# Performance work log

Hardware: AMD Instinct MI355X
Metric: run time of the kernel (lower is better)

The kernel has to match this reference:

```python
import jax, jax.numpy as jnp
import numpy as np
from jax import lax

B, T, DEPTH = 512, 32, 512
RNN, NCC = 512, 128
D_IN = DEPTH * (T * DEPTH // T // DEPTH) * 1 + NCC  # slice_len=1 -> 512 + 128 = 640


def setup_inputs() -> dict:
    key = jax.random.key(0)
    ks = jax.random.split(key, 7)
    s = 0.05  # tf.random_normal_initializer default stddev
    return {
        "f_pool": jax.random.normal(ks[0], (B, T, DEPTH), jnp.float32),
        "ground_truth": jax.random.normal(ks[1], (B, T, NCC), jnp.float32),
        "kernel": jax.random.normal(ks[2], (DEPTH + NCC, 4 * RNN), jnp.float32) * s,
        "rec_kernel": jax.random.normal(ks[3], (RNN, 4 * RNN), jnp.float32) * s,
        "bias": jax.random.normal(ks[4], (4 * RNN,), jnp.float32) * s,
        "softmax_w": jax.random.normal(ks[5], (RNN, NCC), jnp.float32) * s,
        "softmax_b": jax.random.normal(ks[6], (NCC,), jnp.float32) * s,
    }


def reference(f_pool, ground_truth, kernel, rec_kernel, bias, softmax_w, softmax_b):
    b, features_num, depth = f_pool.shape
    seq_length = ground_truth.shape[1]
    ncc = softmax_b.shape[0]
    rnn = rec_kernel.shape[0]
    slice_len = features_num // seq_length  # == 1 here
    gt_t = jnp.transpose(ground_truth, (1, 0, 2))  # [T, B, C] for scan

    def step(carry, inp):
        h, c, prev = carry
        t, gt_row = inp
        # image feature slice at char index t -> [B, slice_len*depth]
        feat = lax.dynamic_slice_in_dim(f_pool, t, slice_len, axis=1)
        feat = feat.reshape(b, slice_len * depth)
        x = jnp.concatenate([feat, prev], axis=1)
        z = x @ kernel + h @ rec_kernel + bias  # [B, 4*rnn]
        i, f, g, o = jnp.split(z, 4, axis=1)    # keras LSTMCell gate order
        c2 = jax.nn.sigmoid(f) * c + jax.nn.sigmoid(i) * jnp.tanh(g)
        h2 = jax.nn.sigmoid(o) * jnp.tanh(c2)
        logits = h2 @ softmax_w + softmax_b
        onehot = jax.nn.one_hot(jnp.argmax(logits, axis=1), ncc, dtype=f_pool.dtype)
        # teacher forcing: prev_output = ground_truth[:, t, :]
        return (h2, c2, gt_row), onehot

    h0 = jnp.zeros((b, rnn), f_pool.dtype)
    c0 = jnp.zeros((b, rnn), f_pool.dtype)
    prev0 = jnp.zeros((b, ncc), f_pool.dtype)
    (h, c, _), outs = lax.scan(step, (h0, c0, prev0), (jnp.arange(seq_length), gt_t))
    sequence_output = jnp.transpose(outs, (1, 0, 2))  # [B, T, C]
    return (sequence_output, h, c)
```

## Files before the change

kernel.cpp:

```cpp
#include <hip/hip_runtime.h>
#include <math.h>

typedef float  f32x4  __attribute__((ext_vector_type(4)));
typedef short  short8v __attribute__((ext_vector_type(8)));
typedef unsigned short ushort8v __attribute__((ext_vector_type(8)));
typedef unsigned short ushort4v __attribute__((ext_vector_type(4)));

#define KP_PRE 3840
#define KP_HS  1536

#define WAITV(N) asm volatile("s_waitcnt vmcnt(" #N ")" ::: "memory")
#define SBAR()   asm volatile("s_barrier" ::: "memory")

__device__ unsigned short g_Xb[16384][3840];
__device__ unsigned short g_Wb[2048][3840];
__device__ unsigned short g_Rb[2048][1536];
__device__ unsigned short g_hs[2][512][1536];
__device__ float g_pre[16384][2048];
__device__ float g_hf[2][512 * 512];
__device__ float g_swT[128][512];
__device__ float g_bperm[2048];
__device__ float g_plv[2][512 * 8];
__device__ int   g_pli[2][512 * 8];
__device__ unsigned g_xcnt[128];
__device__ unsigned g_pcnt[256];
__device__ unsigned g_prel[256];

__global__ void init_counters()
{
    int t = threadIdx.x;
    if (t < 8) g_xcnt[t * 16] = 0u;
    if (t < 4) { g_pcnt[t * 64] = 0u; g_prel[t * 64] = 0u; }
}

__device__ __forceinline__ unsigned short f2bf(float f) {
    unsigned u = __float_as_uint(f);
    return (unsigned short)((u + 0x7fffu + ((u >> 16) & 1u)) >> 16);
}
__device__ __forceinline__ float bf2f(unsigned short s) {
    return __uint_as_float(((unsigned)s) << 16);
}
__device__ __forceinline__ float sigf(float x) { return 1.f / (1.f + expf(-x)); }

__device__ __forceinline__ void split3(float v, unsigned short& s0,
                                       unsigned short& s1, unsigned short& s2) {
    s0 = f2bf(v); float f0 = bf2f(s0);
    s1 = f2bf(v - f0); float f1 = bf2f(s1);
    s2 = f2bf(v - f0 - f1);
}

__device__ __constant__ int c_ipt[6] = {0, 0, 1, 0, 1, 2};
__device__ __constant__ int c_jpt[6] = {0, 1, 0, 2, 1, 0};

__device__ __forceinline__ void gl16(const unsigned short* g, unsigned short* l) {
    __builtin_amdgcn_global_load_lds((const __attribute__((address_space(1))) void*)g,
                                     (__attribute__((address_space(3))) void*)l, 16, 0, 0);
}

__device__ __forceinline__ short8v fragld(const unsigned short* sh, int row, int uw) {
    return *(const short8v*)(sh + row * 64 + ((uw ^ (row & 7)) << 3));
}

template<int AUNITS, int BUNITS>
__device__ __forceinline__ void stage_chunk(const unsigned short* Ag, int pitchA,
                                            const unsigned short* Bg, int pitchB,
                                            int kb, unsigned short* slot, int tid)
{
#pragma unroll
    for (int v = 0; v < AUNITS / 256; ++v) {
        int e = v * 256 + tid;
        gl16(Ag + (size_t)(e >> 3) * pitchA + kb * 64 + (e & 7) * 8, slot + e * 8);
    }
#pragma unroll
    for (int v = 0; v < BUNITS / 256; ++v) {
        int e = v * 256 + tid;
        gl16(Bg + (size_t)(e >> 3) * pitchB + kb * 64 + (e & 7) * 8,
             slot + AUNITS * 8 + e * 8);
    }
}

__device__ __forceinline__ void stageA3(const unsigned short* Ag, int kr,
                                        unsigned short* buf, int tid)
{
#pragma unroll
    for (int s = 0; s < 3; ++s)
#pragma unroll
        for (int v = 0; v < 2; ++v) {
            int e = v * 256 + tid;
            gl16(Ag + (size_t)(e >> 3) * KP_HS + (s * 8 + kr) * 64 + (e & 7) * 8,
                 buf + s * 4096 + e * 8);
        }
}
__device__ __forceinline__ void stageB3(const unsigned short* Bg, int kr,
                                        unsigned short* buf, int tid)
{
#pragma unroll
    for (int s = 0; s < 3; ++s)
#pragma unroll
        for (int v = 0; v < 2; ++v) {
            int e = v * 256 + tid;
            gl16(Bg + (size_t)(e >> 3) * KP_HS + (s * 8 + kr) * 64 + (e & 7) * 8,
                 buf + 12288 + s * 4096 + e * 8);
        }
}
__device__ __forceinline__ void stage6(const unsigned short* Ag,
                                       const unsigned short* Bg,
                                       int kr, unsigned short* buf, int tid)
{
    stageA3(Ag, kr, buf, tid);
    stageB3(Bg, kr, buf, tid);
}

__global__ __launch_bounds__(256) void build_Xb(const float* __restrict__ fp,
                                                const float* __restrict__ gt)
{
    const int tid = threadIdx.x;
    const int m  = blockIdx.x * 16 + (tid >> 4);
    const int k8 = (blockIdx.y * 16 + (tid & 15)) * 8;
    const int t = m >> 9, b = m & 511;
    float x[8];
    if (k8 < 512) {
        float4 v0 = *(const float4*)(fp + ((size_t)(b * 32 + t)) * 512 + k8);
        float4 v1 = *(const float4*)(fp + ((size_t)(b * 32 + t)) * 512 + k8 + 4);
        x[0]=v0.x; x[1]=v0.y; x[2]=v0.z; x[3]=v0.w;
        x[4]=v1.x; x[5]=v1.y; x[6]=v1.z; x[7]=v1.w;
    } else if (t > 0) {
        float4 v0 = *(const float4*)(gt + ((size_t)(b * 32 + t - 1)) * 128 + (k8 - 512));
        float4 v1 = *(const float4*)(gt + ((size_t)(b * 32 + t - 1)) * 128 + (k8 - 512) + 4);
        x[0]=v0.x; x[1]=v0.y; x[2]=v0.z; x[3]=v0.w;
        x[4]=v1.x; x[5]=v1.y; x[6]=v1.z; x[7]=v1.w;
    } else {
#pragma unroll
        for (int j = 0; j < 8; ++j) x[j] = 0.f;
    }
    unsigned short s0[8], s1[8], s2[8];
#pragma unroll
    for (int j = 0; j < 8; ++j) split3(x[j], s0[j], s1[j], s2[j]);
    const int u = (k8 >> 3) & 7;
    const int base = (k8 & ~63) + (((u ^ (m & 7))) << 3);
#pragma unroll
    for (int p = 0; p < 6; ++p) {
        ushort8v v;
#pragma unroll
        for (int j = 0; j < 8; ++j)
            v[j] = (c_ipt[p] == 0) ? s0[j] : ((c_ipt[p] == 1) ? s1[j] : s2[j]);
        *(ushort8v*)&g_Xb[m][p * 640 + base] = v;
    }
}

__global__ __launch_bounds__(256) void build_Wb(const float* __restrict__ Wk)
{
    const int tid = threadIdx.x;
    const int np = blockIdx.x * 16 + (tid >> 4);
    const int k8 = (blockIdx.y * 16 + (tid & 15)) * 8;
    const int n = (np & 3) * 512 + (np >> 2);
    float x[8];
#pragma unroll
    for (int j = 0; j < 8; ++j) x[j] = Wk[(size_t)(k8 + j) * 2048 + n];
    unsigned short s0[8], s1[8], s2[8];
#pragma unroll
    for (int j = 0; j < 8; ++j) split3(x[j], s0[j], s1[j], s2[j]);
    const int u = (k8 >> 3) & 7;
    const int base = (k8 & ~63) + (((u ^ (np & 7))) << 3);
#pragma unroll
    for (int p = 0; p < 6; ++p) {
        ushort8v v;
#pragma unroll
        for (int j = 0; j < 8; ++j)
            v[j] = (c_jpt[p] == 0) ? s0[j] : ((c_jpt[p] == 1) ? s1[j] : s2[j]);
        *(ushort8v*)&g_Wb[np][p * 640 + base] = v;
    }
}

__global__ __launch_bounds__(256) void build_Rb(const float* __restrict__ Rk)
{
    const int tid = threadIdx.x;
    const int np = blockIdx.x * 16 + (tid >> 4);
    const int k8 = (blockIdx.y * 16 + (tid & 15)) * 8;
    const int n = (np & 3) * 512 + (np >> 2);
    float x[8];
#pragma unroll
    for (int j = 0; j < 8; ++j) x[j] = Rk[(size_t)(k8 + j) * 2048 + n];
    unsigned short s0[8], s1[8], s2[8];
#pragma unroll
    for (int j = 0; j < 8; ++j) split3(x[j], s0[j], s1[j], s2[j]);
    const int u = (k8 >> 3) & 7;
    const int base = (k8 & ~63) + (((u ^ (np & 7))) << 3);
    ushort8v v0, v1, v2;
#pragma unroll
    for (int j = 0; j < 8; ++j) { v0[j] = s0[j]; v1[j] = s1[j]; v2[j] = s2[j]; }
    *(ushort8v*)&g_Rb[np][0 * 512 + base] = v0;
    *(ushort8v*)&g_Rb[np][1 * 512 + base] = v1;
    *(ushort8v*)&g_Rb[np][2 * 512 + base] = v2;
}

__global__ __launch_bounds__(256) void build_misc(const float* __restrict__ sw,
                                                  const float* __restrict__ bias)
{
    int id = blockIdx.x * 256 + threadIdx.x;
    if (id < 128 * 512) {
        int c = id >> 9, r = id & 511;
        g_swT[c][r] = sw[(size_t)r * 128 + c];
    } else if (id < 128 * 512 + 2048) {
        int np = id - 128 * 512;
        g_bperm[np] = bias[(np & 3) * 512 + (np >> 2)];
    }
}

__global__ __launch_bounds__(256, 1) void pre_mfma()
{
    __shared__ __align__(16) char smem[98304];
    const int tid = threadIdx.x, lane = tid & 63, wave = tid >> 6;
    const int n0 = blockIdx.x * 64, m0 = blockIdx.y * 128;
    const int wr = wave >> 1, wc = wave & 1, l15 = lane & 15, ql = lane >> 4;
    unsigned short* ring = (unsigned short*)smem;
    const unsigned short* Ag = &g_Xb[m0][0];
    const unsigned short* Bg = &g_Wb[n0][0];

    f32x4 acc[4][2];
#pragma unroll
    for (int a = 0; a < 4; ++a)
#pragma unroll
        for (int b = 0; b < 2; ++b) acc[a][b] = (f32x4){0.f, 0.f, 0.f, 0.f};

    stage_chunk<1024, 512>(Ag, KP_PRE, Bg, KP_PRE, 0, ring + 0 * 12288, tid);
    stage_chunk<1024, 512>(Ag, KP_PRE, Bg, KP_PRE, 1, ring + 1 * 12288, tid);
    stage_chunk<1024, 512>(Ag, KP_PRE, Bg, KP_PRE, 2, ring + 2 * 12288, tid);
    for (int c = 0; c < 60; ++c) {
        if (c <= 57)      WAITV(12);
        else if (c == 58) WAITV(6);
        else              WAITV(0);
        SBAR();
        const unsigned short* Ac = ring + (c & 3) * 12288;
        const unsigned short* Bc = Ac + 8192;
#pragma unroll
        for (int sub = 0; sub < 2; ++sub) {
            const int uw = sub * 4 + ql;
            short8v af[4], bfr[2];
#pragma unroll
            for (int fa = 0; fa < 4; ++fa)
                af[fa] = fragld(Ac, wr * 64 + fa * 16 + l15, uw);
#pragma unroll
            for (int fb = 0; fb < 2; ++fb)
                bfr[fb] = fragld(Bc, wc * 32 + fb * 16 + l15, uw);
#pragma unroll
            for (int fa = 0; fa < 4; ++fa)
#pragma unroll
                for (int fb = 0; fb < 2; ++fb)
                    acc[fa][fb] = __builtin_amdgcn_mfma_f32_16x16x32_bf16(
                        af[fa], bfr[fb], acc[fa][fb], 0, 0, 0);
        }
        if (c + 3 < 60)
            stage_chunk<1024, 512>(Ag, KP_PRE, Bg, KP_PRE, c + 3,
                                   ring + ((c + 3) & 3) * 12288, tid);
    }
#pragma unroll
    for (int fa = 0; fa < 4; ++fa)
#pragma unroll
        for (int fb = 0; fb < 2; ++fb) {
            const int np = n0 + wc * 32 + fb * 16 + l15;
            const float bv = g_bperm[np];
#pragma unroll
            for (int q = 0; q < 4; ++q) {
                const int m = m0 + wr * 64 + fa * 16 + ql * 4 + q;
                g_pre[m][np] = acc[fa][fb][q] + bv;
            }
        }
}

__global__ __launch_bounds__(256, 1) void charnn_rec(
    const float* __restrict__ sb,
    float* __restrict__ seq, float* __restrict__ out_h, float* __restrict__ out_c)
{
    __shared__ __align__(16) char smem[147456];
    float (*zbuf)[68] = (float (*)[68])smem;
    unsigned short* ring = (unsigned short*)smem;

    const int bi = blockIdx.x, tid = threadIdx.x;
    const int lane = tid & 63, wave = tid >> 6;
    const int x  = bi & 7, jj = bi >> 3;
    const int P  = x >> 1, e = x & 1;
    const int Mg = 2 * P + (jj & 1);
    const int Ng = e * 16 + (jj >> 1);
    const int m0 = Mg * 64, n0 = Ng * 64;
    const int wr = wave >> 1, wc = wave & 1, l15 = lane & 15, ql = lane >> 4;

    const int m_e = tid >> 2;
    const int rb4 = (tid & 3) * 4;
    const int mg = m0 + m_e;
    float cst[4] = {0.f, 0.f, 0.f, 0.f};

    const int q    = e * 32 + jj;
    const int rgrp = 8 * P + (q & 7);
    const int cg   = q >> 3;
    const int arow = 128 * P + q * 2;
    const bool xleader = (jj == 0);
    const bool pleader = (jj == 0 && e == 0);

    constexpr int ipt[6] = {0, 0, 1, 0, 1, 2};
    constexpr int jpt[6] = {0, 1, 0, 2, 1, 0};

    const unsigned short* Bg = &g_Rb[n0][0];

    f32x4 pq0, pq1, pq2, pq3;
    {
        const float* prow = &g_pre[0 * 512 + mg][n0];
        pq0 = *(const f32x4*)(prow + rb4 * 4);
        pq1 = *(const f32x4*)(prow + rb4 * 4 + 4);
        pq2 = *(const f32x4*)(prow + rb4 * 4 + 8);
        pq3 = *(const f32x4*)(prow + rb4 * 4 + 12);
    }

    for (int ph = 0; ph < 34; ++ph) {
        const int t = ph;
        const bool do_z = (ph >= 1 && ph <= 31);

        const unsigned short* Ag = nullptr;
        if (do_z) {
            Ag = &g_hs[(t + 1) & 1][m0][0];
            stageA3(Ag, 0, ring + 0 * 24576, tid);
            stageA3(Ag, 1, ring + 1 * 24576, tid);
            stageA3(Ag, 2, ring + 2 * 24576, tid);
        }

        if (ph >= 1 && ph <= 32) {
            const int tl = ph - 1;
            const int row = rgrp * 16 + (tid >> 4);
            const int col = cg * 16 + (tid & 15);
            const float* hrow = &g_hf[tl & 1][(size_t)row * 512];
            const float* wcol = &g_swT[col][0];
            float s0 = sb[col], s1 = 0.f, s2 = 0.f, s3 = 0.f;
#pragma unroll 8
            for (int k = 0; k < 512; k += 4) {
                float4 hv = *(const float4*)(hrow + k);
                float4 wv = *(const float4*)(wcol + k);
                s0 = fmaf(hv.x, wv.x, s0); s1 = fmaf(hv.y, wv.y, s1);
                s2 = fmaf(hv.z, wv.z, s2); s3 = fmaf(hv.w, wv.w, s3);
            }
            float bv = (s0 + s1) + (s2 + s3); int bidx = col;
#pragma unroll
            for (int m = 1; m < 16; m <<= 1) {
                float ov = __shfl_xor(bv, m, 64);
                int   oi = __shfl_xor(bidx, m, 64);
                if (ov > bv || (ov == bv && oi < bidx)) { bv = ov; bidx = oi; }
            }
            if ((tid & 15) == 0) {
                g_plv[tl & 1][row * 8 + cg] = bv;
                g_pli[tl & 1][row * 8 + cg] = bidx;
            }
        }

        if (ph >= 2 && wave < 2) {
            const int t2 = ph - 2;
            const int row = arow + wave;
            float v; int idx;
            if (lane < 8) {
                v   = g_plv[t2 & 1][row * 8 + lane];
                idx = g_pli[t2 & 1][row * 8 + lane];
            } else { v = -INFINITY; idx = 0x7fffffff; }
#pragma unroll
            for (int m = 1; m < 8; m <<= 1) {
                float ov = __shfl_xor(v, m, 64);
                int   oi = __shfl_xor(idx, m, 64);
                if (ov > v || (ov == v && oi < idx)) { v = ov; idx = oi; }
            }
            int win = __shfl(idx, 0, 64);
            if (lane < 32) {
                int c4 = lane * 4;
                float4 o;
                o.x = (c4 + 0 == win) ? 1.f : 0.f;
                o.y = (c4 + 1 == win) ? 1.f : 0.f;
                o.z = (c4 + 2 == win) ? 1.f : 0.f;
                o.w = (c4 + 3 == win) ? 1.f : 0.f;
                *(float4*)(seq + ((size_t)row * 32 + t2) * 128 + c4) = o;
            }
        }

        if (ph <= 31) {
            if (do_z) {
                f32x4 acc[2][2];
#pragma unroll
                for (int a = 0; a < 2; ++a)
#pragma unroll
                    for (int b = 0; b < 2; ++b) acc[a][b] = (f32x4){0.f, 0.f, 0.f, 0.f};
#pragma unroll
                for (int kr = 0; kr < 8; ++kr) {
                    if (kr >= 1 && kr <= 5)
                        stage6(Ag, Bg, kr + 2, ring + ((kr + 2) % 3) * 24576, tid);
                    if      (kr == 0) WAITV(12);
                    else if (kr == 1) WAITV(18);
                    else if (kr == 2) WAITV(24);
                    else if (kr == 3) WAITV(24);
                    else if (kr == 4) WAITV(24);
                    else if (kr == 5) WAITV(24);
                    else if (kr == 6) WAITV(12);
                    else              WAITV(0);
                    SBAR();
                    const unsigned short* Ab = ring + (kr % 3) * 24576;
                    const unsigned short* Bb = Ab + 12288;
#pragma unroll
                    for (int sub = 0; sub < 2; ++sub) {
                        const int uw = sub * 4 + ql;
                        short8v a0[2], a1[2], a2[2], b0[2], b1[2], b2[2];
                        a0[0] = fragld(Ab + 0 * 4096, wr * 32 + l15, uw);
                        a0[1] = fragld(Ab + 0 * 4096, wr * 32 + 16 + l15, uw);
                        a1[0] = fragld(Ab + 1 * 4096, wr * 32 + l15, uw);
                        a1[1] = fragld(Ab + 1 * 4096, wr * 32 + 16 + l15, uw);
                        a2[0] = fragld(Ab + 2 * 4096, wr * 32 + l15, uw);
                        a2[1] = fragld(Ab + 2 * 4096, wr * 32 + 16 + l15, uw);
                        b0[0] = fragld(Bb + 0 * 4096, wc * 32 + l15, uw);
                        b0[1] = fragld(Bb + 0 * 4096, wc * 32 + 16 + l15, uw);
                        b1[0] = fragld(Bb + 1 * 4096, wc * 32 + l15, uw);
                        b1[1] = fragld(Bb + 1 * 4096, wc * 32 + 16 + l15, uw);
                        b2[0] = fragld(Bb + 2 * 4096, wc * 32 + l15, uw);
                        b2[1] = fragld(Bb + 2 * 4096, wc * 32 + 16 + l15, uw);
#pragma unroll
                        for (int p = 0; p < 6; ++p) {
                            const short8v* A2 = (ipt[p] == 0) ? a0 :
                                                ((ipt[p] == 1) ? a1 : a2);
                            const short8v* B2 = (jpt[p] == 0) ? b0 :
                                                ((jpt[p] == 1) ? b1 : b2);
                            acc[0][0] = __builtin_amdgcn_mfma_f32_16x16x32_bf16(
                                A2[0], B2[0], acc[0][0], 0, 0, 0);
                            acc[0][1] = __builtin_amdgcn_mfma_f32_16x16x32_bf16(
                                A2[0], B2[1], acc[0][1], 0, 0, 0);
                            acc[1][0] = __builtin_amdgcn_mfma_f32_16x16x32_bf16(
                                A2[1], B2[0], acc[1][0], 0, 0, 0);
                            acc[1][1] = __builtin_amdgcn_mfma_f32_16x16x32_bf16(
                                A2[1], B2[1], acc[1][1], 0, 0, 0);
                        }
                    }
                }
                __syncthreads();
#pragma unroll
                for (int fa = 0; fa < 2; ++fa)
#pragma unroll
                    for (int fb = 0; fb < 2; ++fb)
#pragma unroll
                        for (int q2 = 0; q2 < 4; ++q2)
                            zbuf[wr * 32 + fa * 16 + ql * 4 + q2]
                                [wc * 32 + fb * 16 + l15] = acc[fa][fb][q2];
            }
            __syncthreads();

            unsigned short hs0[4], hs1[4], hs2[4];
            float hv4[4];
#pragma unroll
            for (int i = 0; i < 4; ++i) {
                const int rl = rb4 + i;
                float zi, zf, zg, zo;
                if (t > 0) {
                    float4 zq = *(const float4*)&zbuf[m_e][rl * 4];
                    zi = zq.x; zf = zq.y; zg = zq.z; zo = zq.w;
                } else { zi = zf = zg = zo = 0.f; }
                f32x4 pq = (i == 0) ? pq0 : ((i == 1) ? pq1 : ((i == 2) ? pq2 : pq3));
                zi += pq[0]; zf += pq[1]; zg += pq[2]; zo += pq[3];
                float c2 = sigf(zf) * cst[i] + sigf(zi) * tanhf(zg);
                float h2 = sigf(zo) * tanhf(c2);
                cst[i] = c2;
                hv4[i] = h2;
                split3(h2, hs0[i], hs1[i], hs2[i]);
            }
            const int r0g = Ng * 16 + rb4;
            *(float4*)&g_hf[t & 1][(size_t)mg * 512 + r0g] =
                make_float4(hv4[0], hv4[1], hv4[2], hv4[3]);
            if (t == 31) {
                *(float4*)&out_h[(size_t)mg * 512 + r0g] =
                    make_float4(hv4[0], hv4[1], hv4[2], hv4[3]);
                *(float4*)&out_c[(size_t)mg * 512 + r0g] =
                    make_float4(cst[0], cst[1], cst[2], cst[3]);
            }
            const int su = ((r0g >> 3) & 7) ^ (mg & 7);
            const int abase = (r0g & ~63) + (su << 3) + (r0g & 7);
#pragma unroll
            for (int i = 0; i < 3; ++i) {
                ushort4v v;
#pragma unroll
                for (int j = 0; j < 4; ++j)
                    v[j] = (i == 0) ? hs0[j] : ((i == 1) ? hs1[j] : hs2[j]);
                *(ushort4v*)&g_hs[t & 1][mg][i * 512 + abase] = v;
            }
        }

        if (ph < 33) {
            __syncthreads();

            if (ph <= 30) {
                stageB3(Bg, 0, ring + 0 * 24576, tid);
                stageB3(Bg, 1, ring + 1 * 24576, tid);
                stageB3(Bg, 2, ring + 2 * 24576, tid);
                const float* prow = &g_pre[(ph + 1) * 512 + mg][n0];
                pq0 = *(const f32x4*)(prow + rb4 * 4);
                pq1 = *(const f32x4*)(prow + rb4 * 4 + 4);
                pq2 = *(const f32x4*)(prow + rb4 * 4 + 8);
                pq3 = *(const f32x4*)(prow + rb4 * 4 + 12);
            }

            if (tid == 0) {
                __hip_atomic_fetch_add(&g_xcnt[x * 16], 1u,
                                       __ATOMIC_RELAXED, __HIP_MEMORY_SCOPE_AGENT);
                if (xleader) {
                    const unsigned xt = 32u * (unsigned)(ph + 1);
                    while (__hip_atomic_load(&g_xcnt[x * 16], __ATOMIC_RELAXED,
                                             __HIP_MEMORY_SCOPE_AGENT) < xt)
                        __builtin_amdgcn_s_sleep(2);
                    __builtin_amdgcn_fence(__ATOMIC_RELEASE, "agent");
                    __hip_atomic_fetch_add(&g_pcnt[P * 64], 1u,
                                           __ATOMIC_RELAXED, __HIP_MEMORY_SCOPE_AGENT);
                    if (pleader) {
                        const unsigned pt = 2u * (unsigned)(ph + 1);
                        while (__hip_atomic_load(&g_pcnt[P * 64], __ATOMIC_RELAXED,
                                                 __HIP_MEMORY_SCOPE_AGENT) < pt)
                            __builtin_amdgcn_s_sleep(2);
                        __hip_atomic_store(&g_prel[P * 64], (unsigned)(ph + 1),
                                           __ATOMIC_RELAXED, __HIP_MEMORY_SCOPE_AGENT);
                    }
                }
                while (__hip_atomic_load(&g_prel[P * 64], __ATOMIC_RELAXED,
                                         __HIP_MEMORY_SCOPE_AGENT) < (unsigned)(ph + 1))
                    __builtin_amdgcn_s_sleep(2);
                __builtin_amdgcn_fence(__ATOMIC_ACQUIRE, "agent");
            }
            __syncthreads();
        }
    }
}

extern "C" void kernel_launch(void* const* d_in, const int* in_sizes, int n_in,
                              void* d_out, int out_size, void* d_ws, size_t ws_size,
                              hipStream_t stream)
{
    const float* fp   = (const float*)d_in[0];
    const float* gt   = (const float*)d_in[1];
    const float* Wk   = (const float*)d_in[2];
    const float* Rk   = (const float*)d_in[3];
    const float* bias = (const float*)d_in[4];
    const float* sw   = (const float*)d_in[5];
    const float* sb   = (const float*)d_in[6];
    float* seq   = (float*)d_out;
    float* out_h = seq + (size_t)512 * 32 * 128;
    float* out_c = out_h + (size_t)512 * 512;

    hipLaunchKernelGGL(init_counters, dim3(1), dim3(64), 0, stream);
    hipLaunchKernelGGL(build_Xb, dim3(1024, 5), dim3(256), 0, stream, fp, gt);
    hipLaunchKernelGGL(build_Wb, dim3(128, 5), dim3(256), 0, stream, Wk);
    hipLaunchKernelGGL(build_Rb, dim3(128, 4), dim3(256), 0, stream, Rk);
    hipLaunchKernelGGL(build_misc, dim3(264), dim3(256), 0, stream, sw, bias);
    hipLaunchKernelGGL(pre_mfma, dim3(32, 128), dim3(256), 0, stream);
    hipLaunchKernelGGL(charnn_rec, dim3(256), dim3(256), 0, stream,
                       sb, seq, out_h, out_c);
}
```

Before: 1.706 ms.

## Regroup recurrent blocks so each batch-row group syncs independently

```diff
diff --git a/kernel.cpp b/kernel.cpp
--- a/kernel.cpp
+++ b/kernel.cpp
@@ -23,14 +23,12 @@
 __device__ float g_plv[2][512 * 8];
 __device__ int   g_pli[2][512 * 8];
 __device__ unsigned g_xcnt[128];
-__device__ unsigned g_pcnt[256];
-__device__ unsigned g_prel[256];
+__device__ unsigned g_xrel[128];
 
 __global__ void init_counters()
 {
     int t = threadIdx.x;
-    if (t < 8) g_xcnt[t * 16] = 0u;
-    if (t < 4) { g_pcnt[t * 64] = 0u; g_prel[t * 64] = 0u; }
+    if (t < 8) { g_xcnt[t * 16] = 0u; g_xrel[t * 16] = 0u; }
 }
 
 __device__ __forceinline__ unsigned short f2bf(float f) {
@@ -279,9 +277,8 @@
     const int bi = blockIdx.x, tid = threadIdx.x;
     const int lane = tid & 63, wave = tid >> 6;
     const int x  = bi & 7, jj = bi >> 3;
-    const int P  = x >> 1, e = x & 1;
-    const int Mg = 2 * P + (jj & 1);
-    const int Ng = e * 16 + (jj >> 1);
+    const int Mg = x;
+    const int Ng = jj;
     const int m0 = Mg * 64, n0 = Ng * 64;
     const int wr = wave >> 1, wc = wave & 1, l15 = lane & 15, ql = lane >> 4;
 
@@ -290,12 +287,10 @@
     const int mg = m0 + m_e;
     float cst[4] = {0.f, 0.f, 0.f, 0.f};
 
-    const int q    = e * 32 + jj;
-    const int rgrp = 8 * P + (q & 7);
-    const int cg   = q >> 3;
-    const int arow = 128 * P + q * 2;
+    const int rgrp = Mg * 4 + (jj & 3);
+    const int cg   = jj >> 2;
+    const int arow = Mg * 64 + jj * 2;
     const bool xleader = (jj == 0);
-    const bool pleader = (jj == 0 && e == 0);
 
     constexpr int ipt[6] = {0, 0, 1, 0, 1, 2};
     constexpr int jpt[6] = {0, 1, 0, 2, 1, 0};
@@ -504,19 +499,10 @@
                     while (__hip_atomic_load(&g_xcnt[x * 16], __ATOMIC_RELAXED,
                                              __HIP_MEMORY_SCOPE_AGENT) < xt)
                         __builtin_amdgcn_s_sleep(2);
-                    __builtin_amdgcn_fence(__ATOMIC_RELEASE, "agent");
-                    __hip_atomic_fetch_add(&g_pcnt[P * 64], 1u,
-                                           __ATOMIC_RELAXED, __HIP_MEMORY_SCOPE_AGENT);
-                    if (pleader) {
-                        const unsigned pt = 2u * (unsigned)(ph + 1);
-                        while (__hip_atomic_load(&g_pcnt[P * 64], __ATOMIC_RELAXED,
-                                                 __HIP_MEMORY_SCOPE_AGENT) < pt)
-                            __builtin_amdgcn_s_sleep(2);
-                        __hip_atomic_store(&g_prel[P * 64], (unsigned)(ph + 1),
-                                           __ATOMIC_RELAXED, __HIP_MEMORY_SCOPE_AGENT);
-                    }
+                    __hip_atomic_store(&g_xrel[x * 16], (unsigned)(ph + 1),
+                                       __ATOMIC_RELAXED, __HIP_MEMORY_SCOPE_AGENT);
                 }
-                while (__hip_atomic_load(&g_prel[P * 64], __ATOMIC_RELAXED,
+                while (__hip_atomic_load(&g_xrel[x * 16], __ATOMIC_RELAXED,
                                          __HIP_MEMORY_SCOPE_AGENT) < (unsigned)(ph + 1))
                     __builtin_amdgcn_s_sleep(2);
                 __builtin_amdgcn_fence(__ATOMIC_ACQUIRE, "agent");
```

After: 1.711 ms. Within noise of the previous version (+0.3%).
